# Performance work log

Hardware: AMD Instinct MI355X
Metric: run time of the kernel (lower is better)

Reference implementation:

```python
import jax, jax.numpy as jnp
import numpy as np

# Standard TCN TemporalBlock (Bai et al.): dilated causal conv -> chomp -> relu ->
# (dropout, identity at eval) x2, plus 1x1-conv residual, final relu.
# PyTorch pads (k-1)*d on both sides then chomps the right, which equals
# left-only causal padding of (k-1)*d.

def _causal_conv(x, w, b, dilation):
    pad = (w.shape[-1] - 1) * dilation
    y = jax.lax.conv_general_dilated(
        x, w, window_strides=(1,), padding=[(pad, 0)],
        rhs_dilation=(dilation,), dimension_numbers=('NCH', 'OIH', 'NCH'))
    return y + b[None, :, None]

def _block(x, w1, b1, w2, b2, wd, bd, dil):
    h = jax.nn.relu(_causal_conv(x, w1, b1, dil))
    h = jax.nn.relu(_causal_conv(h, w2, b2, dil))
    res = _causal_conv(x, wd, bd, 1)  # 1x1 downsample (channel counts differ)
    return jax.nn.relu(h + res)

def setup_inputs() -> dict:
    key = jax.random.key(0)
    ks = jax.random.split(key, 18)
    B, Cin, L, C1, C2, H, K, O = 4096, 30, 256, 100, 200, 8, 5, 1
    def rn(k, shape, s=0.05):
        return jax.random.normal(k, shape, dtype=jnp.float32) * s
    return {
        'x': rn(ks[0], (B, Cin, L), 1.0),
        'task_labels': jax.random.randint(ks[1], (B,), 0, H),
        # TCN level 0: in_features -> 100, dilation 1
        'w1_0': rn(ks[2], (C1, Cin, K)), 'b1_0': rn(ks[3], (C1,)),
        'w2_0': rn(ks[4], (C1, C1, K)),  'b2_0': rn(ks[5], (C1,)),
        'wd_0': rn(ks[6], (C1, Cin, 1)), 'bd_0': rn(ks[7], (C1,)),
        # TCN level 1: 100 -> 200, dilation 2
        'w1_1': rn(ks[8], (C2, C1, K)),  'b1_1': rn(ks[9], (C2,)),
        'w2_1': rn(ks[10], (C2, C2, K)), 'b2_1': rn(ks[11], (C2,)),
        'wd_1': rn(ks[12], (C2, C1, 1)), 'bd_1': rn(ks[13], (C2,)),
        # 8 per-task heads, stacked: Linear(200->100), Tanh, Linear(100->1)
        'hw1': rn(ks[14], (H, C1, C2)), 'hb1': rn(ks[15], (H, C1)),
        'hw2': rn(ks[16], (H, O, C1)),  'hb2': rn(ks[17], (H, O)),
    }

def reference(x, task_labels, w1_0, b1_0, w2_0, b2_0, wd_0, bd_0,
              w1_1, b1_1, w2_1, b2_1, wd_1, bd_1, hw1, hb1, hw2, hb2):
    # TCN backbone (eval mode: dropout is identity)
    y = _block(x, w1_0, b1_0, w2_0, b2_0, wd_0, bd_0, 1)
    y = _block(y, w1_1, b1_1, w2_1, b2_1, wd_1, bd_1, 2)
    feat = y[:, :, -1]  # [B, 200] last timestep
    # Vectorized per-task head dispatch: gather each sample's head weights.
    # Mathematically identical to the per-task gather/MLP/scatter loop.
    W1 = hw1[task_labels]  # [B, 100, 200]
    B1 = hb1[task_labels]  # [B, 100]
    W2 = hw2[task_labels]  # [B, 1, 100]
    B2 = hb2[task_labels]  # [B, 1]
    h = jnp.tanh(jnp.einsum('bd,bod->bo', feat, W1) + B1)
    return jnp.einsum('bo,bpo->bp', h, W2) + B2  # [B, 1]
```

## Files before the change

kernel.cpp:

```cpp
#include <hip/hip_runtime.h>
#include <math.h>


#define R     4096
#define CIN   30
#define LSEQ  256
#define C1    100
#define C2    200
#define KW    5
#define T0    231
#define WIN   25
#define NU0   21
#define NJ0   9
#define NT1   5

#define ROW_XT    0
#define ROW_H0T   750
#define ROW_Y0T   2850
#define ROW_H1T   0
#define ROW_FEAT  3750

__global__ __launch_bounds__(1024) void k_tr(const float* __restrict__ x,
                                             float* __restrict__ xT) {
  const int l = threadIdx.x & 63;
  const int wv = threadIdx.x >> 6;
  const int b = blockIdx.x * 64 + l;
  const float* xb = x + (size_t)b * (CIN * LSEQ) + T0;
  for (int r = wv; r < CIN * WIN; r += 16) {
    const int ci = r / WIN;
    const int u = r - ci * WIN;
    xT[(size_t)r * R + b] = xb[ci * LSEQ + u];
  }
}

__global__ __launch_bounds__(256) void k1(const float* __restrict__ xT,
                                          const float* __restrict__ w1,
                                          const float* __restrict__ b1,
                                          float* __restrict__ h0T) {
  __shared__ float wT[CIN * KW * 16];
  const int tid = threadIdx.x;
  const int ctile = blockIdx.y * 16;
  for (int idx = tid; idx < CIN * KW * 16; idx += 256) {
    const int kk = idx >> 4, cl = idx & 15, c = ctile + cl;
    wT[idx] = (c < C1) ? w1[c * (CIN * KW) + kk] : 0.f;
  }
  __syncthreads();
  const int l = tid & 63, wv = tid >> 6;
  const int b = blockIdx.x * 64 + l;
  const int cb = ctile + wv * 4;
  float acc[4][NU0];
#pragma unroll
  for (int m = 0; m < 4; ++m) {
    const float bias = (cb + m < C1) ? b1[cb + m] : 0.f;
#pragma unroll
    for (int u = 0; u < NU0; ++u) acc[m][u] = bias;
  }
  for (int ci = 0; ci < CIN; ++ci) {
    float xr[WIN];
    const float* xp = xT + (size_t)ci * WIN * R + b;
#pragma unroll
    for (int u = 0; u < WIN; ++u) xr[u] = xp[(size_t)u * R];
#pragma unroll
    for (int k = 0; k < KW; ++k) {
      const float4 w = *reinterpret_cast<const float4*>(&wT[(ci * KW + k) * 16 + wv * 4]);
#pragma unroll
      for (int u = 0; u < NU0; ++u) {
        acc[0][u] = fmaf(xr[u + k], w.x, acc[0][u]);
        acc[1][u] = fmaf(xr[u + k], w.y, acc[1][u]);
        acc[2][u] = fmaf(xr[u + k], w.z, acc[2][u]);
        acc[3][u] = fmaf(xr[u + k], w.w, acc[3][u]);
      }
    }
  }
#pragma unroll
  for (int m = 0; m < 4; ++m) {
    const int c = cb + m;
    if (c < C1) {
#pragma unroll
      for (int u = 0; u < NU0; ++u)
        h0T[(size_t)(c * NU0 + u) * R + b] = fmaxf(acc[m][u], 0.f);
    }
  }
}

__global__ __launch_bounds__(256) void k2(const float* __restrict__ xT,
                                          const float* __restrict__ h0T,
                                          const float* __restrict__ w2,
                                          const float* __restrict__ b2,
                                          const float* __restrict__ wd,
                                          const float* __restrict__ bd,
                                          float* __restrict__ y0T) {
  __shared__ float wT[C1 * KW * 16];
  __shared__ float wdT[CIN * 16];
  const int tid = threadIdx.x;
  const int ctile = blockIdx.y * 16;
  for (int idx = tid; idx < C1 * KW * 16; idx += 256) {
    const int kk = idx >> 4, cl = idx & 15, c = ctile + cl;
    wT[idx] = (c < C1) ? w2[c * (C1 * KW) + kk] : 0.f;
  }
  for (int idx = tid; idx < CIN * 16; idx += 256) {
    const int ci = idx >> 4, cl = idx & 15, c = ctile + cl;
    wdT[idx] = (c < C1) ? wd[c * CIN + ci] : 0.f;
  }
  __syncthreads();
  const int l = tid & 63, wv = tid >> 6;
  const int b = blockIdx.x * 64 + l;
  const int cb = ctile + wv * 4;
  float acc[4][NJ0], rac[4][NJ0];
#pragma unroll
  for (int m = 0; m < 4; ++m) {
    const float bias = (cb + m < C1) ? b2[cb + m] : 0.f;
    const float bres = (cb + m < C1) ? bd[cb + m] : 0.f;
#pragma unroll
    for (int j = 0; j < NJ0; ++j) { acc[m][j] = bias; rac[m][j] = bres; }
  }
  for (int ci = 0; ci < C1; ++ci) {
    float hr[NU0];
    const float* hp = h0T + (size_t)ci * NU0 * R + b;
#pragma unroll
    for (int u = 0; u < NU0; ++u) hr[u] = hp[(size_t)u * R];
#pragma unroll
    for (int k = 0; k < KW; ++k) {
      const float4 w = *reinterpret_cast<const float4*>(&wT[(ci * KW + k) * 16 + wv * 4]);
#pragma unroll
      for (int j = 0; j < NJ0; ++j) {
        acc[0][j] = fmaf(hr[2 * j + k], w.x, acc[0][j]);
        acc[1][j] = fmaf(hr[2 * j + k], w.y, acc[1][j]);
        acc[2][j] = fmaf(hr[2 * j + k], w.z, acc[2][j]);
        acc[3][j] = fmaf(hr[2 * j + k], w.w, acc[3][j]);
      }
    }
  }
  for (int ci = 0; ci < CIN; ++ci) {
    float xr[NJ0];
    const float* xp = xT + (size_t)(ci * WIN + 8) * R + b;
#pragma unroll
    for (int j = 0; j < NJ0; ++j) xr[j] = xp[(size_t)(2 * j) * R];
    const float4 w = *reinterpret_cast<const float4*>(&wdT[ci * 16 + wv * 4]);
#pragma unroll
    for (int j = 0; j < NJ0; ++j) {
      rac[0][j] = fmaf(xr[j], w.x, rac[0][j]);
      rac[1][j] = fmaf(xr[j], w.y, rac[1][j]);
      rac[2][j] = fmaf(xr[j], w.z, rac[2][j]);
      rac[3][j] = fmaf(xr[j], w.w, rac[3][j]);
    }
  }
#pragma unroll
  for (int m = 0; m < 4; ++m) {
    const int c = cb + m;
    if (c < C1) {
#pragma unroll
      for (int j = 0; j < NJ0; ++j)
        y0T[(size_t)(c * NJ0 + j) * R + b] =
            fmaxf(fmaxf(acc[m][j], 0.f) + rac[m][j], 0.f);
    }
  }
}

__global__ __launch_bounds__(256) void k3(const float* __restrict__ y0T,
                                          const float* __restrict__ w1,
                                          const float* __restrict__ b1,
                                          float* __restrict__ h1T) {
  __shared__ float wT[C1 * KW * 16];
  const int tid = threadIdx.x;
  const int ctile = blockIdx.y * 16;
  for (int idx = tid; idx < C1 * KW * 16; idx += 256) {
    const int kk = idx >> 4, cl = idx & 15, c = ctile + cl;
    wT[idx] = (c < C2) ? w1[c * (C1 * KW) + kk] : 0.f;
  }
  __syncthreads();
  const int l = tid & 63, wv = tid >> 6;
  const int b = blockIdx.x * 64 + l;
  const int cb = ctile + wv * 4;
  float acc[4][NT1];
#pragma unroll
  for (int m = 0; m < 4; ++m) {
    const float bias = (cb + m < C2) ? b1[cb + m] : 0.f;
#pragma unroll
    for (int t = 0; t < NT1; ++t) acc[m][t] = bias;
  }
  for (int ci = 0; ci < C1; ++ci) {
    float yr[NJ0];
    const float* yp = y0T + (size_t)ci * NJ0 * R + b;
#pragma unroll
    for (int u = 0; u < NJ0; ++u) yr[u] = yp[(size_t)u * R];
#pragma unroll
    for (int k = 0; k < KW; ++k) {
      const float4 w = *reinterpret_cast<const float4*>(&wT[(ci * KW + k) * 16 + wv * 4]);
#pragma unroll
      for (int t = 0; t < NT1; ++t) {
        acc[0][t] = fmaf(yr[t + k], w.x, acc[0][t]);
        acc[1][t] = fmaf(yr[t + k], w.y, acc[1][t]);
        acc[2][t] = fmaf(yr[t + k], w.z, acc[2][t]);
        acc[3][t] = fmaf(yr[t + k], w.w, acc[3][t]);
      }
    }
  }
#pragma unroll
  for (int m = 0; m < 4; ++m) {
    const int c = cb + m;
    if (c < C2) {
#pragma unroll
      for (int t = 0; t < NT1; ++t)
        h1T[(size_t)(c * NT1 + t) * R + b] = fmaxf(acc[m][t], 0.f);
    }
  }
}

__global__ __launch_bounds__(256) void k4a(const float* __restrict__ h1T,
                                           const float* __restrict__ y0T,
                                           const float* __restrict__ w2,
                                           const float* __restrict__ b2,
                                           const float* __restrict__ wd,
                                           const float* __restrict__ bd,
                                           float* __restrict__ featT) {
  __shared__ float wT[C2 * KW * 8];
  __shared__ float wdT[C1 * 8];
  const int tid = threadIdx.x;
  const int cb8 = blockIdx.y * 8;
  for (int idx = tid; idx < C2 * KW * 8; idx += 256) {
    const int kk = idx >> 3, cl = idx & 7;
    wT[idx] = w2[(cb8 + cl) * (C2 * KW) + kk];
  }
  for (int idx = tid; idx < C1 * 8; idx += 256) {
    const int ci = idx >> 3, cl = idx & 7;
    wdT[idx] = wd[(cb8 + cl) * C1 + ci];
  }
  __syncthreads();
  const int l = tid & 63, wv = tid >> 6;
  const int b4 = blockIdx.x * 256 + l * 4;
  const int c0 = cb8 + wv * 2;
  float a0[4], a1[4], r0[4], r1[4];
  {
    const float bA = b2[c0], bB = b2[c0 + 1];
    const float dA = bd[c0], dB = bd[c0 + 1];
#pragma unroll
    for (int m = 0; m < 4; ++m) { a0[m] = bA; a1[m] = bB; r0[m] = dA; r1[m] = dB; }
  }
#pragma unroll 4
  for (int kk = 0; kk < C2 * KW; ++kk) {
    const float4 h = *reinterpret_cast<const float4*>(&h1T[(size_t)kk * R + b4]);
    const float2 w = *reinterpret_cast<const float2*>(&wT[kk * 8 + wv * 2]);
    a0[0] = fmaf(h.x, w.x, a0[0]); a0[1] = fmaf(h.y, w.x, a0[1]);
    a0[2] = fmaf(h.z, w.x, a0[2]); a0[3] = fmaf(h.w, w.x, a0[3]);
    a1[0] = fmaf(h.x, w.y, a1[0]); a1[1] = fmaf(h.y, w.y, a1[1]);
    a1[2] = fmaf(h.z, w.y, a1[2]); a1[3] = fmaf(h.w, w.y, a1[3]);
  }
#pragma unroll 4
  for (int ci = 0; ci < C1; ++ci) {
    const float4 y = *reinterpret_cast<const float4*>(&y0T[(size_t)(ci * NJ0 + 8) * R + b4]);
    const float2 w = *reinterpret_cast<const float2*>(&wdT[ci * 8 + wv * 2]);
    r0[0] = fmaf(y.x, w.x, r0[0]); r0[1] = fmaf(y.y, w.x, r0[1]);
    r0[2] = fmaf(y.z, w.x, r0[2]); r0[3] = fmaf(y.w, w.x, r0[3]);
    r1[0] = fmaf(y.x, w.y, r1[0]); r1[1] = fmaf(y.y, w.y, r1[1]);
    r1[2] = fmaf(y.z, w.y, r1[2]); r1[3] = fmaf(y.w, w.y, r1[3]);
  }
  float4 f0, f1;
  f0.x = fmaxf(fmaxf(a0[0], 0.f) + r0[0], 0.f);
  f0.y = fmaxf(fmaxf(a0[1], 0.f) + r0[1], 0.f);
  f0.z = fmaxf(fmaxf(a0[2], 0.f) + r0[2], 0.f);
  f0.w = fmaxf(fmaxf(a0[3], 0.f) + r0[3], 0.f);
  f1.x = fmaxf(fmaxf(a1[0], 0.f) + r1[0], 0.f);
  f1.y = fmaxf(fmaxf(a1[1], 0.f) + r1[1], 0.f);
  f1.z = fmaxf(fmaxf(a1[2], 0.f) + r1[2], 0.f);
  f1.w = fmaxf(fmaxf(a1[3], 0.f) + r1[3], 0.f);
  *reinterpret_cast<float4*>(&featT[(size_t)c0 * R + b4]) = f0;
  *reinterpret_cast<float4*>(&featT[(size_t)(c0 + 1) * R + b4]) = f1;
}

__global__ __launch_bounds__(256) void k4b(const float* __restrict__ featT,
                                           const int* __restrict__ labels,
                                           const float* __restrict__ hw1,
                                           const float* __restrict__ hb1,
                                           const float* __restrict__ hw2,
                                           const float* __restrict__ hb2,
                                           float* __restrict__ out) {
  __shared__ float fs[4][C2];
  const int tid = threadIdx.x;
  const int b0 = blockIdx.x * 4;
  for (int idx = tid; idx < 4 * C2; idx += 256) {
    const int c = idx >> 2, bi = idx & 3;
    fs[bi][c] = featT[(size_t)c * R + b0 + bi];
  }
  __syncthreads();
  const int l = tid & 63, wv = tid >> 6;
  const int b = b0 + wv;
  const int task = labels[b];
  const float* W1 = hw1 + (size_t)task * (C1 * C2);
  const float* fp = fs[wv];
  float p = 0.f;
  {
    float a = hb1[task * C1 + l];
    const float* wr = W1 + (size_t)l * C2;
#pragma unroll 4
    for (int d = 0; d < C2; d += 4) {
      const float4 fv = *reinterpret_cast<const float4*>(&fp[d]);
      const float4 wv4 = *reinterpret_cast<const float4*>(&wr[d]);
      a = fmaf(fv.x, wv4.x, a); a = fmaf(fv.y, wv4.y, a);
      a = fmaf(fv.z, wv4.z, a); a = fmaf(fv.w, wv4.w, a);
    }
    p = tanhf(a) * hw2[task * C1 + l];
  }
  if (l < C1 - 64) {
    const int o = 64 + l;
    float a = hb1[task * C1 + o];
    const float* wr = W1 + (size_t)o * C2;
#pragma unroll 4
    for (int d = 0; d < C2; d += 4) {
      const float4 fv = *reinterpret_cast<const float4*>(&fp[d]);
      const float4 wv4 = *reinterpret_cast<const float4*>(&wr[d]);
      a = fmaf(fv.x, wv4.x, a); a = fmaf(fv.y, wv4.y, a);
      a = fmaf(fv.z, wv4.z, a); a = fmaf(fv.w, wv4.w, a);
    }
    p = fmaf(tanhf(a), hw2[task * C1 + o], p);
  }
#pragma unroll
  for (int off = 32; off > 0; off >>= 1) p += __shfl_down(p, off, 64);
  if (l == 0) out[b] = p + hb2[task];
}

extern "C" void kernel_launch(void* const* d_in, const int* in_sizes, int n_in,
                              void* d_out, int out_size, void* d_ws, size_t ws_size,
                              hipStream_t stream) {
  const float* x    = (const float*)d_in[0];
  const int* labels = (const int*)d_in[1];
  const float* w1_0 = (const float*)d_in[2];
  const float* b1_0 = (const float*)d_in[3];
  const float* w2_0 = (const float*)d_in[4];
  const float* b2_0 = (const float*)d_in[5];
  const float* wd_0 = (const float*)d_in[6];
  const float* bd_0 = (const float*)d_in[7];
  const float* w1_1 = (const float*)d_in[8];
  const float* b1_1 = (const float*)d_in[9];
  const float* w2_1 = (const float*)d_in[10];
  const float* b2_1 = (const float*)d_in[11];
  const float* wd_1 = (const float*)d_in[12];
  const float* bd_1 = (const float*)d_in[13];
  const float* hw1  = (const float*)d_in[14];
  const float* hb1  = (const float*)d_in[15];
  const float* hw2  = (const float*)d_in[16];
  const float* hb2  = (const float*)d_in[17];
  float* out = (float*)d_out;

  float* ws    = (float*)d_ws;
  float* xT    = ws + (size_t)ROW_XT * R;
  float* h0T   = ws + (size_t)ROW_H0T * R;
  float* y0T   = ws + (size_t)ROW_Y0T * R;
  float* h1T   = ws + (size_t)ROW_H1T * R;
  float* featT = ws + (size_t)ROW_FEAT * R;

  hipLaunchKernelGGL(k_tr, dim3(64), dim3(1024), 0, stream, x, xT);
  hipLaunchKernelGGL(k1, dim3(64, 7), dim3(256), 0, stream, xT, w1_0, b1_0, h0T);
  hipLaunchKernelGGL(k2, dim3(64, 7), dim3(256), 0, stream, xT, h0T, w2_0, b2_0, wd_0, bd_0, y0T);
  hipLaunchKernelGGL(k3, dim3(64, 13), dim3(256), 0, stream, y0T, w1_1, b1_1, h1T);
  hipLaunchKernelGGL(k4a, dim3(16, 25), dim3(256), 0, stream, h1T, y0T, w2_1, b2_1, wd_1, bd_1, featT);
  hipLaunchKernelGGL(k4b, dim3(1024), dim3(256), 0, stream, featT, labels,
                     hw1, hb1, hw2, hb2, out);
}
```

Baseline: 596.3 us.

## Pre-transpose weights in a prep kernel and shrink per-wave channel tiles for more blocks

Adds a prep kernel that writes channel-contiguous copies of all conv weights and the head W1 into workspace. The conv kernels then read weights straight from global memory with wave-uniform scalar loads instead of staging them in LDS. Each wave now handles 2 channels (8 per block) instead of 4, giving many more blocks (1D grid), and k4a drops its float4 batch vectorization. The head kernel reads transposed W1 rows so lanes access coalesced memory. The cost is an extra launch, rewriting ~2MB of weights on every call, and re-reading activations once per smaller channel tile, which means more global traffic.

```diff
diff --git a/kernel.cpp b/kernel.cpp
--- a/kernel.cpp
+++ b/kernel.cpp
@@ -14,263 +14,235 @@
 #define NJ0   9
 #define NT1   5
 
-#define ROW_XT    0
-#define ROW_H0T   750
-#define ROW_Y0T   2850
-#define ROW_H1T   0
-#define ROW_FEAT  3750
-
-__global__ __launch_bounds__(1024) void k_tr(const float* __restrict__ x,
-                                             float* __restrict__ xT) {
-  const int l = threadIdx.x & 63;
-  const int wv = threadIdx.x >> 6;
+#define OFF_HW1T  0
+#define OFF_WT10  160000
+#define OFF_WT20  175000
+#define OFF_WDT0  225000
+#define OFF_WT11  228000
+#define OFF_WT21  328000
+#define OFF_WDT1  528000
+#define ROW_XT    134
+#define ROW_H0T   884
+#define ROW_Y0T   2984
+#define ROW_H1T   134
+#define ROW_FEAT  1134
+
+#define NPREP 548000
+__global__ __launch_bounds__(256) void k_prep(
+    const float* __restrict__ hw1, const float* __restrict__ w1_0,
+    const float* __restrict__ w2_0, const float* __restrict__ wd_0,
+    const float* __restrict__ w1_1, const float* __restrict__ w2_1,
+    const float* __restrict__ wd_1, float* __restrict__ ws) {
+  int idx = blockIdx.x * 256 + threadIdx.x;
+  if (idx >= NPREP) return;
+  if (idx < 160000) {
+    const int h = idx / 20000, r = idx - h * 20000;
+    const int d = r / C1, o = r - d * C1;
+    ws[OFF_HW1T + idx] = hw1[h * 20000 + o * C2 + d];
+  } else if (idx < 175000) {
+    const int r = idx - 160000, kk = r / C1, c = r - kk * C1;
+    ws[idx] = w1_0[c * (CIN * KW) + kk];
+  } else if (idx < 225000) {
+    const int r = idx - 175000, kk = r / C1, c = r - kk * C1;
+    ws[idx] = w2_0[c * (C1 * KW) + kk];
+  } else if (idx < 228000) {
+    const int r = idx - 225000, ci = r / C1, c = r - ci * C1;
+    ws[idx] = wd_0[c * CIN + ci];
+  } else if (idx < 328000) {
+    const int r = idx - 228000, kk = r / C2, c = r - kk * C2;
+    ws[idx] = w1_1[c * (C1 * KW) + kk];
+  } else if (idx < 528000) {
+    const int r = idx - 328000, kk = r / C2, c = r - kk * C2;
+    ws[idx] = w2_1[(size_t)c * (C2 * KW) + kk];
+  } else {
+    const int r = idx - 528000, ci = r / C2, c = r - ci * C2;
+    ws[idx] = wd_1[c * C1 + ci];
+  }
+}
+
+__global__ __launch_bounds__(256) void k_tr(const float* __restrict__ x,
+                                            float* __restrict__ xT) {
+  const int l = threadIdx.x & 63, wv = threadIdx.x >> 6;
   const int b = blockIdx.x * 64 + l;
   const float* xb = x + (size_t)b * (CIN * LSEQ) + T0;
-  for (int r = wv; r < CIN * WIN; r += 16) {
-    const int ci = r / WIN;
-    const int u = r - ci * WIN;
+  for (int r2 = wv; r2 < 150; r2 += 4) {
+    const int r = blockIdx.y * 150 + r2;
+    const int ci = r / WIN, u = r - ci * WIN;
     xT[(size_t)r * R + b] = xb[ci * LSEQ + u];
   }
 }
 
 __global__ __launch_bounds__(256) void k1(const float* __restrict__ xT,
-                                          const float* __restrict__ w1,
+                                          const float* __restrict__ wT10,
                                           const float* __restrict__ b1,
                                           float* __restrict__ h0T) {
-  __shared__ float wT[CIN * KW * 16];
-  const int tid = threadIdx.x;
-  const int ctile = blockIdx.y * 16;
-  for (int idx = tid; idx < CIN * KW * 16; idx += 256) {
-    const int kk = idx >> 4, cl = idx & 15, c = ctile + cl;
-    wT[idx] = (c < C1) ? w1[c * (CIN * KW) + kk] : 0.f;
-  }
-  __syncthreads();
-  const int l = tid & 63, wv = tid >> 6;
-  const int b = blockIdx.x * 64 + l;
-  const int cb = ctile + wv * 4;
-  float acc[4][NU0];
-#pragma unroll
-  for (int m = 0; m < 4; ++m) {
-    const float bias = (cb + m < C1) ? b1[cb + m] : 0.f;
-#pragma unroll
-    for (int u = 0; u < NU0; ++u) acc[m][u] = bias;
-  }
+  const int id = blockIdx.x;
+  const int bblk = id & 63, ct = id >> 6;
+  const int tid = threadIdx.x;
+  const int l = tid & 63, wv = tid >> 6;
+  const int b = bblk * 64 + l;
+  int c0 = ct * 8 + __builtin_amdgcn_readfirstlane(wv) * 2;
+  c0 = (c0 > C1 - 2) ? C1 - 2 : c0;
+  float acc0[NU0], acc1[NU0];
+  const float bi0 = b1[c0], bi1 = b1[c0 + 1];
+#pragma unroll
+  for (int u = 0; u < NU0; ++u) { acc0[u] = bi0; acc1[u] = bi1; }
   for (int ci = 0; ci < CIN; ++ci) {
     float xr[WIN];
-    const float* xp = xT + (size_t)ci * WIN * R + b;
-#pragma unroll
-    for (int u = 0; u < WIN; ++u) xr[u] = xp[(size_t)u * R];
+#pragma unroll
+    for (int u = 0; u < WIN; ++u) xr[u] = xT[(size_t)(ci * WIN + u) * R + b];
 #pragma unroll
     for (int k = 0; k < KW; ++k) {
-      const float4 w = *reinterpret_cast<const float4*>(&wT[(ci * KW + k) * 16 + wv * 4]);
+      const float* wr = wT10 + (ci * KW + k) * C1 + c0;
+      const float w0 = wr[0], w1v = wr[1];
 #pragma unroll
       for (int u = 0; u < NU0; ++u) {
-        acc[0][u] = fmaf(xr[u + k], w.x, acc[0][u]);
-        acc[1][u] = fmaf(xr[u + k], w.y, acc[1][u]);
-        acc[2][u] = fmaf(xr[u + k], w.z, acc[2][u]);
-        acc[3][u] = fmaf(xr[u + k], w.w, acc[3][u]);
+        acc0[u] = fmaf(xr[u + k], w0, acc0[u]);
+        acc1[u] = fmaf(xr[u + k], w1v, acc1[u]);
       }
     }
   }
 #pragma unroll
-  for (int m = 0; m < 4; ++m) {
-    const int c = cb + m;
-    if (c < C1) {
-#pragma unroll
-      for (int u = 0; u < NU0; ++u)
-        h0T[(size_t)(c * NU0 + u) * R + b] = fmaxf(acc[m][u], 0.f);
-    }
+  for (int u = 0; u < NU0; ++u) {
+    h0T[(size_t)(c0 * NU0 + u) * R + b] = fmaxf(acc0[u], 0.f);
+    h0T[(size_t)((c0 + 1) * NU0 + u) * R + b] = fmaxf(acc1[u], 0.f);
   }
 }
 
 __global__ __launch_bounds__(256) void k2(const float* __restrict__ xT,
                                           const float* __restrict__ h0T,
-                                          const float* __restrict__ w2,
+                                          const float* __restrict__ wT20,
                                           const float* __restrict__ b2,
-                                          const float* __restrict__ wd,
+                                          const float* __restrict__ wdT0,
                                           const float* __restrict__ bd,
                                           float* __restrict__ y0T) {
-  __shared__ float wT[C1 * KW * 16];
-  __shared__ float wdT[CIN * 16];
-  const int tid = threadIdx.x;
-  const int ctile = blockIdx.y * 16;
-  for (int idx = tid; idx < C1 * KW * 16; idx += 256) {
-    const int kk = idx >> 4, cl = idx & 15, c = ctile + cl;
-    wT[idx] = (c < C1) ? w2[c * (C1 * KW) + kk] : 0.f;
-  }
-  for (int idx = tid; idx < CIN * 16; idx += 256) {
-    const int ci = idx >> 4, cl = idx & 15, c = ctile + cl;
-    wdT[idx] = (c < C1) ? wd[c * CIN + ci] : 0.f;
-  }
-  __syncthreads();
-  const int l = tid & 63, wv = tid >> 6;
-  const int b = blockIdx.x * 64 + l;
-  const int cb = ctile + wv * 4;
-  float acc[4][NJ0], rac[4][NJ0];
-#pragma unroll
-  for (int m = 0; m < 4; ++m) {
-    const float bias = (cb + m < C1) ? b2[cb + m] : 0.f;
-    const float bres = (cb + m < C1) ? bd[cb + m] : 0.f;
-#pragma unroll
-    for (int j = 0; j < NJ0; ++j) { acc[m][j] = bias; rac[m][j] = bres; }
-  }
-  for (int ci = 0; ci < C1; ++ci) {
-    float hr[NU0];
-    const float* hp = h0T + (size_t)ci * NU0 * R + b;
-#pragma unroll
-    for (int u = 0; u < NU0; ++u) hr[u] = hp[(size_t)u * R];
-#pragma unroll
-    for (int k = 0; k < KW; ++k) {
-      const float4 w = *reinterpret_cast<const float4*>(&wT[(ci * KW + k) * 16 + wv * 4]);
-#pragma unroll
-      for (int j = 0; j < NJ0; ++j) {
-        acc[0][j] = fmaf(hr[2 * j + k], w.x, acc[0][j]);
-        acc[1][j] = fmaf(hr[2 * j + k], w.y, acc[1][j]);
-        acc[2][j] = fmaf(hr[2 * j + k], w.z, acc[2][j]);
-        acc[3][j] = fmaf(hr[2 * j + k], w.w, acc[3][j]);
-      }
-    }
-  }
-  for (int ci = 0; ci < CIN; ++ci) {
-    float xr[NJ0];
-    const float* xp = xT + (size_t)(ci * WIN + 8) * R + b;
-#pragma unroll
-    for (int j = 0; j < NJ0; ++j) xr[j] = xp[(size_t)(2 * j) * R];
-    const float4 w = *reinterpret_cast<const float4*>(&wdT[ci * 16 + wv * 4]);
-#pragma unroll
-    for (int j = 0; j < NJ0; ++j) {
-      rac[0][j] = fmaf(xr[j], w.x, rac[0][j]);
-      rac[1][j] = fmaf(xr[j], w.y, rac[1][j]);
-      rac[2][j] = fmaf(xr[j], w.z, rac[2][j]);
-      rac[3][j] = fmaf(xr[j], w.w, rac[3][j]);
-    }
-  }
-#pragma unroll
-  for (int m = 0; m < 4; ++m) {
-    const int c = cb + m;
-    if (c < C1) {
-#pragma unroll
-      for (int j = 0; j < NJ0; ++j)
-        y0T[(size_t)(c * NJ0 + j) * R + b] =
-            fmaxf(fmaxf(acc[m][j], 0.f) + rac[m][j], 0.f);
-    }
-  }
-}
-
-__global__ __launch_bounds__(256) void k3(const float* __restrict__ y0T,
-                                          const float* __restrict__ w1,
-                                          const float* __restrict__ b1,
-                                          float* __restrict__ h1T) {
-  __shared__ float wT[C1 * KW * 16];
-  const int tid = threadIdx.x;
-  const int ctile = blockIdx.y * 16;
-  for (int idx = tid; idx < C1 * KW * 16; idx += 256) {
-    const int kk = idx >> 4, cl = idx & 15, c = ctile + cl;
-    wT[idx] = (c < C2) ? w1[c * (C1 * KW) + kk] : 0.f;
-  }
-  __syncthreads();
-  const int l = tid & 63, wv = tid >> 6;
-  const int b = blockIdx.x * 64 + l;
-  const int cb = ctile + wv * 4;
-  float acc[4][NT1];
-#pragma unroll
-  for (int m = 0; m < 4; ++m) {
-    const float bias = (cb + m < C2) ? b1[cb + m] : 0.f;
-#pragma unroll
-    for (int t = 0; t < NT1; ++t) acc[m][t] = bias;
-  }
-  for (int ci = 0; ci < C1; ++ci) {
-    float yr[NJ0];
-    const float* yp = y0T + (size_t)ci * NJ0 * R + b;
-#pragma unroll
-    for (int u = 0; u < NJ0; ++u) yr[u] = yp[(size_t)u * R];
-#pragma unroll
-    for (int k = 0; k < KW; ++k) {
-      const float4 w = *reinterpret_cast<const float4*>(&wT[(ci * KW + k) * 16 + wv * 4]);
-#pragma unroll
-      for (int t = 0; t < NT1; ++t) {
-        acc[0][t] = fmaf(yr[t + k], w.x, acc[0][t]);
-        acc[1][t] = fmaf(yr[t + k], w.y, acc[1][t]);
-        acc[2][t] = fmaf(yr[t + k], w.z, acc[2][t]);
-        acc[3][t] = fmaf(yr[t + k], w.w, acc[3][t]);
-      }
-    }
-  }
-#pragma unroll
-  for (int m = 0; m < 4; ++m) {
-    const int c = cb + m;
-    if (c < C2) {
-#pragma unroll
-      for (int t = 0; t < NT1; ++t)
-        h1T[(size_t)(c * NT1 + t) * R + b] = fmaxf(acc[m][t], 0.f);
-    }
-  }
-}
-
-__global__ __launch_bounds__(256) void k4a(const float* __restrict__ h1T,
-                                           const float* __restrict__ y0T,
-                                           const float* __restrict__ w2,
-                                           const float* __restrict__ b2,
-                                           const float* __restrict__ wd,
-                                           const float* __restrict__ bd,
-                                           float* __restrict__ featT) {
-  __shared__ float wT[C2 * KW * 8];
-  __shared__ float wdT[C1 * 8];
-  const int tid = threadIdx.x;
-  const int cb8 = blockIdx.y * 8;
-  for (int idx = tid; idx < C2 * KW * 8; idx += 256) {
-    const int kk = idx >> 3, cl = idx & 7;
-    wT[idx] = w2[(cb8 + cl) * (C2 * KW) + kk];
-  }
-  for (int idx = tid; idx < C1 * 8; idx += 256) {
-    const int ci = idx >> 3, cl = idx & 7;
-    wdT[idx] = wd[(cb8 + cl) * C1 + ci];
-  }
-  __syncthreads();
-  const int l = tid & 63, wv = tid >> 6;
-  const int b4 = blockIdx.x * 256 + l * 4;
-  const int c0 = cb8 + wv * 2;
-  float a0[4], a1[4], r0[4], r1[4];
+  const int id = blockIdx.x;
+  const int bblk = id & 63, ct = id >> 6;
+  const int tid = threadIdx.x;
+  const int l = tid & 63, wv = tid >> 6;
+  const int b = bblk * 64 + l;
+  int c0 = ct * 8 + __builtin_amdgcn_readfirstlane(wv) * 2;
+  c0 = (c0 > C1 - 2) ? C1 - 2 : c0;
+  float acc0[NJ0], acc1[NJ0], rac0[NJ0], rac1[NJ0];
   {
     const float bA = b2[c0], bB = b2[c0 + 1];
     const float dA = bd[c0], dB = bd[c0 + 1];
 #pragma unroll
-    for (int m = 0; m < 4; ++m) { a0[m] = bA; a1[m] = bB; r0[m] = dA; r1[m] = dB; }
-  }
+    for (int j = 0; j < NJ0; ++j) { acc0[j] = bA; acc1[j] = bB; rac0[j] = dA; rac1[j] = dB; }
+  }
+  for (int ci = 0; ci < CIN; ++ci) {
+    float xr[NJ0];
+#pragma unroll
+    for (int j = 0; j < NJ0; ++j) xr[j] = xT[(size_t)(ci * WIN + 8 + 2 * j) * R + b];
+    const float* wr = wdT0 + ci * C1 + c0;
+    const float w0 = wr[0], w1v = wr[1];
+#pragma unroll
+    for (int j = 0; j < NJ0; ++j) {
+      rac0[j] = fmaf(xr[j], w0, rac0[j]);
+      rac1[j] = fmaf(xr[j], w1v, rac1[j]);
+    }
+  }
+  for (int ci = 0; ci < C1; ++ci) {
+    float hr[NU0];
+#pragma unroll
+    for (int u = 0; u < NU0; ++u) hr[u] = h0T[(size_t)(ci * NU0 + u) * R + b];
+#pragma unroll
+    for (int k = 0; k < KW; ++k) {
+      const float* wr = wT20 + (ci * KW + k) * C1 + c0;
+      const float w0 = wr[0], w1v = wr[1];
+#pragma unroll
+      for (int j = 0; j < NJ0; ++j) {
+        acc0[j] = fmaf(hr[2 * j + k], w0, acc0[j]);
+        acc1[j] = fmaf(hr[2 * j + k], w1v, acc1[j]);
+      }
+    }
+  }
+#pragma unroll
+  for (int j = 0; j < NJ0; ++j) {
+    y0T[(size_t)(c0 * NJ0 + j) * R + b] = fmaxf(fmaxf(acc0[j], 0.f) + rac0[j], 0.f);
+    y0T[(size_t)((c0 + 1) * NJ0 + j) * R + b] = fmaxf(fmaxf(acc1[j], 0.f) + rac1[j], 0.f);
+  }
+}
+
+__global__ __launch_bounds__(256) void k3(const float* __restrict__ y0T,
+                                          const float* __restrict__ wT11,
+                                          const float* __restrict__ b1,
+                                          float* __restrict__ h1T) {
+  const int id = blockIdx.x;
+  const int bblk = id & 63, ct = id >> 6;
+  const int tid = threadIdx.x;
+  const int l = tid & 63, wv = tid >> 6;
+  const int b = bblk * 64 + l;
+  const int c0 = ct * 8 + __builtin_amdgcn_readfirstlane(wv) * 2;
+  float acc0[NT1], acc1[NT1];
+  const float bi0 = b1[c0], bi1 = b1[c0 + 1];
+#pragma unroll
+  for (int t = 0; t < NT1; ++t) { acc0[t] = bi0; acc1[t] = bi1; }
+  for (int ci = 0; ci < C1; ++ci) {
+    float yr[NJ0];
+#pragma unroll
+    for (int u = 0; u < NJ0; ++u) yr[u] = y0T[(size_t)(ci * NJ0 + u) * R + b];
+#pragma unroll
+    for (int k = 0; k < KW; ++k) {
+      const float* wr = wT11 + (ci * KW + k) * C2 + c0;
+      const float w0 = wr[0], w1v = wr[1];
+#pragma unroll
+      for (int t = 0; t < NT1; ++t) {
+        acc0[t] = fmaf(yr[t + k], w0, acc0[t]);
+        acc1[t] = fmaf(yr[t + k], w1v, acc1[t]);
+      }
+    }
+  }
+#pragma unroll
+  for (int t = 0; t < NT1; ++t) {
+    h1T[(size_t)(c0 * NT1 + t) * R + b] = fmaxf(acc0[t], 0.f);
+    h1T[(size_t)((c0 + 1) * NT1 + t) * R + b] = fmaxf(acc1[t], 0.f);
+  }
+}
+
+__global__ __launch_bounds__(256) void k4a(const float* __restrict__ h1T,
+                                           const float* __restrict__ y0T,
+                                           const float* __restrict__ wT21,
+                                           const float* __restrict__ b2,
+                                           const float* __restrict__ wdT1,
+                                           const float* __restrict__ bd,
+                                           float* __restrict__ featT) {
+  const int id = blockIdx.x;
+  const int bblk = id & 63, ct = id >> 6;
+  const int tid = threadIdx.x;
+  const int l = tid & 63, wv = tid >> 6;
+  const int b = bblk * 64 + l;
+  int c0 = ct * 32 + __builtin_amdgcn_readfirstlane(wv) * 8;
+  c0 = (c0 > C2 - 8) ? C2 - 8 : c0;
+  float acc[8], rs[8];
+#pragma unroll
+  for (int m = 0; m < 8; ++m) { acc[m] = b2[c0 + m]; rs[m] = bd[c0 + m]; }
 #pragma unroll 4
   for (int kk = 0; kk < C2 * KW; ++kk) {
-    const float4 h = *reinterpret_cast<const float4*>(&h1T[(size_t)kk * R + b4]);
-    const float2 w = *reinterpret_cast<const float2*>(&wT[kk * 8 + wv * 2]);
-    a0[0] = fmaf(h.x, w.x, a0[0]); a0[1] = fmaf(h.y, w.x, a0[1]);
-    a0[2] = fmaf(h.z, w.x, a0[2]); a0[3] = fmaf(h.w, w.x, a0[3]);
-    a1[0] = fmaf(h.x, w.y, a1[0]); a1[1] = fmaf(h.y, w.y, a1[1]);
-    a1[2] = fmaf(h.z, w.y, a1[2]); a1[3] = fmaf(h.w, w.y, a1[3]);
+    const float a = h1T[(size_t)kk * R + b];
+    const float* wr = wT21 + kk * C2 + c0;
+    acc[0] = fmaf(a, wr[0], acc[0]); acc[1] = fmaf(a, wr[1], acc[1]);
+    acc[2] = fmaf(a, wr[2], acc[2]); acc[3] = fmaf(a, wr[3], acc[3]);
+    acc[4] = fmaf(a, wr[4], acc[4]); acc[5] = fmaf(a, wr[5], acc[5]);
+    acc[6] = fmaf(a, wr[6], acc[6]); acc[7] = fmaf(a, wr[7], acc[7]);
   }
 #pragma unroll 4
   for (int ci = 0; ci < C1; ++ci) {
-    const float4 y = *reinterpret_cast<const float4*>(&y0T[(size_t)(ci * NJ0 + 8) * R + b4]);
-    const float2 w = *reinterpret_cast<const float2*>(&wdT[ci * 8 + wv * 2]);
-    r0[0] = fmaf(y.x, w.x, r0[0]); r0[1] = fmaf(y.y, w.x, r0[1]);
-    r0[2] = fmaf(y.z, w.x, r0[2]); r0[3] = fmaf(y.w, w.x, r0[3]);
-    r1[0] = fmaf(y.x, w.y, r1[0]); r1[1] = fmaf(y.y, w.y, r1[1]);
-    r1[2] = fmaf(y.z, w.y, r1[2]); r1[3] = fmaf(y.w, w.y, r1[3]);
-  }
-  float4 f0, f1;
-  f0.x = fmaxf(fmaxf(a0[0], 0.f) + r0[0], 0.f);
-  f0.y = fmaxf(fmaxf(a0[1], 0.f) + r0[1], 0.f);
-  f0.z = fmaxf(fmaxf(a0[2], 0.f) + r0[2], 0.f);
-  f0.w = fmaxf(fmaxf(a0[3], 0.f) + r0[3], 0.f);
-  f1.x = fmaxf(fmaxf(a1[0], 0.f) + r1[0], 0.f);
-  f1.y = fmaxf(fmaxf(a1[1], 0.f) + r1[1], 0.f);
-  f1.z = fmaxf(fmaxf(a1[2], 0.f) + r1[2], 0.f);
-  f1.w = fmaxf(fmaxf(a1[3], 0.f) + r1[3], 0.f);
-  *reinterpret_cast<float4*>(&featT[(size_t)c0 * R + b4]) = f0;
-  *reinterpret_cast<float4*>(&featT[(size_t)(c0 + 1) * R + b4]) = f1;
+    const float a = y0T[(size_t)(ci * NJ0 + 8) * R + b];
+    const float* wr = wdT1 + ci * C2 + c0;
+    rs[0] = fmaf(a, wr[0], rs[0]); rs[1] = fmaf(a, wr[1], rs[1]);
+    rs[2] = fmaf(a, wr[2], rs[2]); rs[3] = fmaf(a, wr[3], rs[3]);
+    rs[4] = fmaf(a, wr[4], rs[4]); rs[5] = fmaf(a, wr[5], rs[5]);
+    rs[6] = fmaf(a, wr[6], rs[6]); rs[7] = fmaf(a, wr[7], rs[7]);
+  }
+#pragma unroll
+  for (int m = 0; m < 8; ++m)
+    featT[(size_t)(c0 + m) * R + b] = fmaxf(fmaxf(acc[m], 0.f) + rs[m], 0.f);
 }
 
 __global__ __launch_bounds__(256) void k4b(const float* __restrict__ featT,
                                            const int* __restrict__ labels,
-                                           const float* __restrict__ hw1,
+                                           const float* __restrict__ hw1T,
                                            const float* __restrict__ hb1,
                                            const float* __restrict__ hw2,
                                            const float* __restrict__ hb2,
@@ -286,34 +258,18 @@
   const int l = tid & 63, wv = tid >> 6;
   const int b = b0 + wv;
   const int task = labels[b];
-  const float* W1 = hw1 + (size_t)task * (C1 * C2);
+  const float* Wt = hw1T + (size_t)task * (C1 * C2);
   const float* fp = fs[wv];
-  float p = 0.f;
-  {
-    float a = hb1[task * C1 + l];
-    const float* wr = W1 + (size_t)l * C2;
-#pragma unroll 4
-    for (int d = 0; d < C2; d += 4) {
-      const float4 fv = *reinterpret_cast<const float4*>(&fp[d]);
-      const float4 wv4 = *reinterpret_cast<const float4*>(&wr[d]);
-      a = fmaf(fv.x, wv4.x, a); a = fmaf(fv.y, wv4.y, a);
-      a = fmaf(fv.z, wv4.z, a); a = fmaf(fv.w, wv4.w, a);
-    }
-    p = tanhf(a) * hw2[task * C1 + l];
-  }
-  if (l < C1 - 64) {
-    const int o = 64 + l;
-    float a = hb1[task * C1 + o];
-    const float* wr = W1 + (size_t)o * C2;
-#pragma unroll 4
-    for (int d = 0; d < C2; d += 4) {
-      const float4 fv = *reinterpret_cast<const float4*>(&fp[d]);
-      const float4 wv4 = *reinterpret_cast<const float4*>(&wr[d]);
-      a = fmaf(fv.x, wv4.x, a); a = fmaf(fv.y, wv4.y, a);
-      a = fmaf(fv.z, wv4.z, a); a = fmaf(fv.w, wv4.w, a);
-    }
-    p = fmaf(tanhf(a), hw2[task * C1 + o], p);
-  }
+  float a0 = hb1[task * C1 + l];
+  float a1 = (l < C1 - 64) ? hb1[task * C1 + 64 + l] : 0.f;
+  for (int d = 0; d < C2; ++d) {
+    const float fd = fp[d];
+    const float* row = Wt + d * C1;
+    a0 = fmaf(fd, row[l], a0);
+    if (l < C1 - 64) a1 = fmaf(fd, row[64 + l], a1);
+  }
+  float p = tanhf(a0) * hw2[task * C1 + l];
+  if (l < C1 - 64) p = fmaf(tanhf(a1), hw2[task * C1 + 64 + l], p);
 #pragma unroll
   for (int off = 32; off > 0; off >>= 1) p += __shfl_down(p, off, 64);
   if (l == 0) out[b] = p + hb2[task];
@@ -343,17 +299,26 @@
   float* out = (float*)d_out;
 
   float* ws    = (float*)d_ws;
+  float* hw1T  = ws + OFF_HW1T;
+  float* wT10  = ws + OFF_WT10;
+  float* wT20  = ws + OFF_WT20;
+  float* wdT0  = ws + OFF_WDT0;
+  float* wT11  = ws + OFF_WT11;
+  float* wT21  = ws + OFF_WT21;
+  float* wdT1  = ws + OFF_WDT1;
   float* xT    = ws + (size_t)ROW_XT * R;
   float* h0T   = ws + (size_t)ROW_H0T * R;
   float* y0T   = ws + (size_t)ROW_Y0T * R;
   float* h1T   = ws + (size_t)ROW_H1T * R;
   float* featT = ws + (size_t)ROW_FEAT * R;
 
-  hipLaunchKernelGGL(k_tr, dim3(64), dim3(1024), 0, stream, x, xT);
-  hipLaunchKernelGGL(k1, dim3(64, 7), dim3(256), 0, stream, xT, w1_0, b1_0, h0T);
-  hipLaunchKernelGGL(k2, dim3(64, 7), dim3(256), 0, stream, xT, h0T, w2_0, b2_0, wd_0, bd_0, y0T);
-  hipLaunchKernelGGL(k3, dim3(64, 13), dim3(256), 0, stream, y0T, w1_1, b1_1, h1T);
-  hipLaunchKernelGGL(k4a, dim3(16, 25), dim3(256), 0, stream, h1T, y0T, w2_1, b2_1, wd_1, bd_1, featT);
+  hipLaunchKernelGGL(k_prep, dim3((NPREP + 255) / 256), dim3(256), 0, stream,
+                     hw1, w1_0, w2_0, wd_0, w1_1, w2_1, wd_1, ws);
+  hipLaunchKernelGGL(k_tr, dim3(64, 5), dim3(256), 0, stream, x, xT);
+  hipLaunchKernelGGL(k1, dim3(13 * 64), dim3(256), 0, stream, xT, wT10, b1_0, h0T);
+  hipLaunchKernelGGL(k2, dim3(13 * 64), dim3(256), 0, stream, xT, h0T, wT20, b2_0, wdT0, bd_0, y0T);
+  hipLaunchKernelGGL(k3, dim3(25 * 64), dim3(256), 0, stream, y0T, wT11, b1_1, h1T);
+  hipLaunchKernelGGL(k4a, dim3(7 * 64), dim3(256), 0, stream, h1T, y0T, wT21, b2_1, wdT1, bd_1, featT);
   hipLaunchKernelGGL(k4b, dim3(1024), dim3(256), 0, stream, featT, labels,
-                     hw1, hb1, hw2, hb2, out);
-}
+                     hw1T, hb1, hw2, hb2, out);
+}
```

Result: slower. 618.5 us (+3.7%).
